# Performance work log

Measured on AMD Instinct MI355X. Metric: run time of the kernel, lower is better.

The kernel has to match this reference:

```python
import jax, jax.numpy as jnp
import numpy as np

D_MODEL = 1024
H = 16
D_K = D_MODEL // H


def setup_inputs() -> dict:
    key = jax.random.key(0)
    ks = jax.random.split(key, 12)
    B, S = 2, 2048
    q = jax.random.normal(ks[0], (B, S, D_MODEL), dtype=jnp.float32)
    k = jax.random.normal(ks[1], (B, S, D_MODEL), dtype=jnp.float32)
    v = jax.random.normal(ks[2], (B, S, D_MODEL), dtype=jnp.float32)
    mask = jax.random.randint(ks[3], (1, 1, S, S), 0, 2, dtype=jnp.int32)
    sc = 1.0 / np.sqrt(D_MODEL)
    wq = jax.random.uniform(ks[4], (D_MODEL, D_MODEL), jnp.float32, -sc, sc)
    bq = jax.random.uniform(ks[5], (D_MODEL,), jnp.float32, -sc, sc)
    wk = jax.random.uniform(ks[6], (D_MODEL, D_MODEL), jnp.float32, -sc, sc)
    bk = jax.random.uniform(ks[7], (D_MODEL,), jnp.float32, -sc, sc)
    wv = jax.random.uniform(ks[8], (D_MODEL, D_MODEL), jnp.float32, -sc, sc)
    bv = jax.random.uniform(ks[9], (D_MODEL,), jnp.float32, -sc, sc)
    wo = jax.random.uniform(ks[10], (D_MODEL, D_MODEL), jnp.float32, -sc, sc)
    bo = jax.random.uniform(ks[11], (D_MODEL,), jnp.float32, -sc, sc)
    return {"q": q, "k": k, "v": v, "mask": mask,
            "wq": wq, "bq": bq, "wk": wk, "bk": bk,
            "wv": wv, "bv": bv, "wo": wo, "bo": bo}


def reference(q, k, v, mask, wq, bq, wk, bk, wv, bv, wo, bo):
    B, S, _ = q.shape
    # linear projections (torch Linear: x @ W.T + b)
    query = q @ wq.T + bq
    key = k @ wk.T + bk
    value = v @ wv.T + bv
    # [B, S, D] -> [B, H, S, d_k]
    query = query.reshape(B, S, H, D_K).transpose(0, 2, 1, 3)
    key = key.reshape(B, S, H, D_K).transpose(0, 2, 1, 3)
    value = value.reshape(B, S, H, D_K).transpose(0, 2, 1, 3)
    scores = jnp.einsum('bhqd,bhkd->bhqk', query, key) / jnp.sqrt(
        jnp.asarray(D_K, query.dtype))
    # NOTE: source uses `-1 ** 9` which is -1 in Python, not -1e9 (soft mask)
    scores = jnp.where(mask == 0, jnp.asarray(-1.0, scores.dtype), scores)
    attn = jax.nn.softmax(scores, axis=-1)
    # source calls dropout(attn) but discards the result -> no-op
    x = jnp.einsum('bhqk,bhkd->bhqd', attn, value)
    x = x.transpose(0, 2, 1, 3).reshape(B, S, H * D_K)
    return x @ wo.T + bo
```

## Files before the change

kernel.cpp:

```cpp
#include <hip/hip_runtime.h>
#include <hip/hip_bf16.h>

#define D_MODEL 1024
#define NH 16
#define DK 64
#define S_LEN 2048
#define BATCH 2
#define M_ROWS (BATCH * S_LEN)

typedef float    floatx4 __attribute__((ext_vector_type(4)));
typedef _Float16 half8   __attribute__((ext_vector_type(8)));
typedef _Float16 half4v  __attribute__((ext_vector_type(4)));

__device__ __forceinline__ half8 ldh8(const _Float16* p) {
    return __builtin_bit_cast(half8, *(const uint4*)p);
}
__device__ __forceinline__ void gld16(const void* g, void* l) {
    __builtin_amdgcn_global_load_lds(
        (const __attribute__((address_space(1))) void*)g,
        (__attribute__((address_space(3))) void*)l, 16, 0, 0);
}

__global__ __launch_bounds__(256)
void cast_h(const float* __restrict__ s0, const float* __restrict__ s1,
            const float* __restrict__ s2, const float* __restrict__ s3,
            _Float16* __restrict__ out, int R) {
    const int z = blockIdx.y;
    const float* src = (z == 0) ? s0 : (z == 1) ? s1 : (z == 2) ? s2 : s3;
    const size_t idx = ((size_t)blockIdx.x * 256 + threadIdx.x) * 4;
    float4 v = *(const float4*)&src[idx];
    half4v h = {(_Float16)v.x, (_Float16)v.y, (_Float16)v.z, (_Float16)v.w};
    *(half4v*)&out[(size_t)z * R * 1024 + idx] = h;
}

template <int OUTMODE>
__global__ __launch_bounds__(256)
void gemm_f16(const _Float16* __restrict__ Abase, const _Float16* __restrict__ Wbase,
              const float* __restrict__ b0, const float* __restrict__ b1,
              const float* __restrict__ b2, void* __restrict__ Obase) {
    __shared__ __align__(16) _Float16 As[128 * 64];
    __shared__ __align__(16) _Float16 Ws[128 * 64];
    const int tid = threadIdx.x;
    const int w = tid >> 6, lane = tid & 63;
    const int l15 = lane & 15, q4 = lane >> 4;
    const int z = (OUTMODE == 1) ? blockIdx.z : 0;
    const int m0 = blockIdx.y * 128, n0 = blockIdx.x * 128;
    const int wm = w >> 1, wn = w & 1;

    const _Float16* A = Abase + (size_t)z * M_ROWS * 1024;
    const _Float16* W = Wbase + (size_t)z * 1024 * 1024;
    const float* bias = (OUTMODE == 1) ? ((z == 0) ? b0 : (z == 1) ? b1 : b2) : b0;

    int srow[4], sseg[4];
#pragma unroll
    for (int i = 0; i < 4; i++) {
        const int slot = i * 256 + tid;
        srow[i] = slot >> 3;
        sseg[i] = ((slot & 7) ^ (srow[i] & 7)) * 8;
    }

    int aoff[4][2], woff[4][2];
#pragma unroll
    for (int r = 0; r < 4; r++) {
        const int ar = wm * 64 + r * 16 + l15;
        const int wr = wn * 64 + r * 16 + l15;
#pragma unroll
        for (int kc = 0; kc < 2; kc++) {
            aoff[r][kc] = (ar * 8 + ((kc * 4 + q4) ^ (ar & 7))) * 8;
            woff[r][kc] = (wr * 8 + ((kc * 4 + q4) ^ (wr & 7))) * 8;
        }
    }

    floatx4 acc[4][4];
#pragma unroll
    for (int r = 0; r < 4; r++)
#pragma unroll
        for (int c = 0; c < 4; c++) acc[r][c] = (floatx4){0.f, 0.f, 0.f, 0.f};

    for (int k0 = 0; k0 < 1024; k0 += 64) {
#pragma unroll
        for (int i = 0; i < 4; i++) {
            const int lb = (i * 256 + w * 64) * 8;
            gld16(&A[(size_t)(m0 + srow[i]) * 1024 + k0 + sseg[i]], &As[lb]);
            gld16(&W[(size_t)(n0 + srow[i]) * 1024 + k0 + sseg[i]], &Ws[lb]);
        }
        __syncthreads();

        half8 af[4][2], wf[4][2];
#pragma unroll
        for (int r = 0; r < 4; r++)
#pragma unroll
            for (int kc = 0; kc < 2; kc++) {
                af[r][kc] = ldh8(&As[aoff[r][kc]]);
                wf[r][kc] = ldh8(&Ws[woff[r][kc]]);
            }
#pragma unroll
        for (int kc = 0; kc < 2; kc++)
#pragma unroll
            for (int r = 0; r < 4; r++)
#pragma unroll
                for (int c = 0; c < 4; c++)
                    acc[r][c] = __builtin_amdgcn_mfma_f32_16x16x32_f16(
                        af[r][kc], wf[c][kc], acc[r][c], 0, 0, 0);
        __syncthreads();
    }

#pragma unroll
    for (int r = 0; r < 4; r++)
#pragma unroll
        for (int c = 0; c < 4; c++)
#pragma unroll
            for (int reg = 0; reg < 4; reg++) {
                const int m = m0 + wm * 64 + r * 16 + q4 * 4 + reg;
                const int n = n0 + wn * 64 + c * 16 + l15;
                float val = acc[r][c][reg] + bias[n];
                if (OUTMODE == 0) {
                    ((float*)Obase)[(size_t)m * 1024 + n] = val;
                } else {
                    if (z == 0) val *= 0.125f;
                    const int b = m >> 11, s = m & 2047;
                    const int h = n >> 6, d = n & 63;
                    _Float16* Oz = (_Float16*)Obase + (size_t)z * M_ROWS * 1024;
                    Oz[(((size_t)(b * 16 + h) * S_LEN + s) << 6) + d] = (_Float16)val;
                }
            }
}

__global__ __launch_bounds__(256)
void vt_trans(const short* __restrict__ Vh, short* __restrict__ Vt) {
    __shared__ __align__(16) short T[64][80];
    const int bh = blockIdx.y;
    const int s0 = blockIdx.x * 64;
    const int t = threadIdx.x;
#pragma unroll
    for (int i = 0; i < 2; i++) {
        const int p = t + i * 256, r = p >> 3, c8 = (p & 7) * 8;
        uint4 raw = *(const uint4*)&Vh[((size_t)bh * S_LEN + s0 + r) * 64 + c8];
        const short* sv = (const short*)&raw;
#pragma unroll
        for (int j = 0; j < 8; j++) T[c8 + j][r] = sv[j];
    }
    __syncthreads();
#pragma unroll
    for (int i = 0; i < 2; i++) {
        const int p = t + i * 256, d = p >> 3, seg = (p & 7) * 8;
        *(uint4*)&Vt[((size_t)bh * DK + d) * S_LEN + s0 + seg] =
            *(const uint4*)&T[d][seg];
    }
}

__global__ __launch_bounds__(256)
void mask_pack(const int* __restrict__ mask, unsigned long long* __restrict__ mb) {
    const int gw = blockIdx.x * 4 + (threadIdx.x >> 6);
    const int lane = threadIdx.x & 63;
    const int row = gw >> 5, wid = gw & 31;
    const int mv = mask[(size_t)row * S_LEN + wid * 64 + lane];
    unsigned long long bal = __ballot(mv != 0);
    if (lane == 0) mb[gw] = bal;
}

__global__ __launch_bounds__(256)
void attn_mfma(const _Float16* __restrict__ Qh, const _Float16* __restrict__ Kh,
               const _Float16* __restrict__ Vt, const unsigned long long* __restrict__ mb,
               _Float16* __restrict__ Xh) {
    __shared__ __align__(16) _Float16 Ks[64 * 72];
    __shared__ __align__(16) _Float16 Vs[64 * 72];
    __shared__ __align__(16) _Float16 Ps[4][16 * 72];

    const int tid = threadIdx.x;
    const int w = tid >> 6, lane = tid & 63;
    const int l15 = lane & 15, q4 = lane >> 4;
    const int bh = blockIdx.y, b = bh >> 4, h = bh & 15;
    const int qb = blockIdx.x * 64 + w * 16;

    const _Float16* Qg = Qh + ((size_t)bh * S_LEN + qb) * DK;
    const _Float16* Kg = Kh + (size_t)bh * S_LEN * DK;
    const _Float16* Vg = Vt + (size_t)bh * DK * S_LEN;

    half8 Aq[2];
#pragma unroll
    for (int c = 0; c < 2; c++)
        Aq[c] = ldh8(&Qg[l15 * DK + c * 32 + q4 * 8]);

    floatx4 O[4];
#pragma unroll
    for (int nt = 0; nt < 4; nt++) O[nt] = (floatx4){0.f, 0.f, 0.f, 0.f};
    float lsum[4] = {0.f, 0.f, 0.f, 0.f};

    for (int j0 = 0; j0 < S_LEN; j0 += 64) {
#pragma unroll
        for (int i = 0; i < 2; i++) {
            int p = tid + i * 256, r = p >> 3, seg = (p & 7) * 8;
            *(uint4*)&Ks[r * 72 + seg] = *(const uint4*)&Kg[(size_t)(j0 + r) * DK + seg];
            *(uint4*)&Vs[r * 72 + seg] = *(const uint4*)&Vg[(size_t)r * S_LEN + j0 + seg];
        }
        unsigned long long mw[4];
#pragma unroll
        for (int reg = 0; reg < 4; reg++)
            mw[reg] = mb[(size_t)(qb + q4 * 4 + reg) * (S_LEN / 64) + (j0 >> 6)];
        __syncthreads();

        floatx4 Sf[4];
#pragma unroll
        for (int jt = 0; jt < 4; jt++) {
            floatx4 c = {0.f, 0.f, 0.f, 0.f};
#pragma unroll
            for (int ch = 0; ch < 2; ch++) {
                half8 bk = ldh8(&Ks[(jt * 16 + l15) * 72 + ch * 32 + q4 * 8]);
                c = __builtin_amdgcn_mfma_f32_16x16x32_f16(Aq[ch], bk, c, 0, 0, 0);
            }
            Sf[jt] = c;
        }

#pragma unroll
        for (int reg = 0; reg < 4; reg++) {
#pragma unroll
            for (int jt = 0; jt < 4; jt++) {
                float s = Sf[jt][reg];
                s = ((mw[reg] >> (jt * 16 + l15)) & 1ull) ? s : -1.0f;
                float p = __expf(s);
                lsum[reg] += p;
                Ps[w][(q4 * 4 + reg) * 72 + jt * 16 + l15] = (_Float16)p;
            }
        }

        half8 Ap[2];
#pragma unroll
        for (int ch = 0; ch < 2; ch++)
            Ap[ch] = ldh8(&Ps[w][l15 * 72 + ch * 32 + q4 * 8]);
#pragma unroll
        for (int nt = 0; nt < 4; nt++) {
#pragma unroll
            for (int ch = 0; ch < 2; ch++) {
                half8 bv = ldh8(&Vs[(nt * 16 + l15) * 72 + ch * 32 + q4 * 8]);
                O[nt] = __builtin_amdgcn_mfma_f32_16x16x32_f16(Ap[ch], bv, O[nt], 0, 0, 0);
            }
        }
        __syncthreads();
    }

#pragma unroll
    for (int reg = 0; reg < 4; reg++) {
#pragma unroll
        for (int off = 1; off < 16; off <<= 1)
            lsum[reg] += __shfl_xor(lsum[reg], off, 64);
    }
#pragma unroll
    for (int reg = 0; reg < 4; reg++) {
        const float inv = 1.0f / lsum[reg];
        const int srow = qb + q4 * 4 + reg;
#pragma unroll
        for (int nt = 0; nt < 4; nt++)
            Xh[((size_t)(b * S_LEN + srow)) * 1024 + h * DK + nt * 16 + l15] =
                (_Float16)(O[nt][reg] * inv);
    }
}

extern "C" void kernel_launch(void* const* d_in, const int* in_sizes, int n_in,
                              void* d_out, int out_size, void* d_ws, size_t ws_size,
                              hipStream_t stream) {
    const float* q  = (const float*)d_in[0];
    const float* k  = (const float*)d_in[1];
    const float* v  = (const float*)d_in[2];
    const int* mask = (const int*)d_in[3];
    const float* wq = (const float*)d_in[4];
    const float* bq = (const float*)d_in[5];
    const float* wk = (const float*)d_in[6];
    const float* bk = (const float*)d_in[7];
    const float* wv = (const float*)d_in[8];
    const float* bv = (const float*)d_in[9];
    const float* wo = (const float*)d_in[10];
    const float* bo = (const float*)d_in[11];
    float* out = (float*)d_out;

    char* ws = (char*)d_ws;
    const size_t MB = 1u << 20;
    _Float16* Wh   = (_Float16*)ws;
    _Float16* Ah   = (_Float16*)(ws + 8 * MB);
    _Float16* QKVh = (_Float16*)(ws + 32 * MB);
    _Float16* Vt   = (_Float16*)(ws + 56 * MB);
    unsigned long long* mb = (unsigned long long*)(ws + 64 * MB);
    _Float16* Xh   = Ah;

    cast_h<<<dim3(1024, 4), 256, 0, stream>>>(wq, wk, wv, wo, Wh, 1024);
    cast_h<<<dim3(4096, 3), 256, 0, stream>>>(q, k, v, nullptr, Ah, M_ROWS);

    gemm_f16<1><<<dim3(8, 32, 3), 256, 0, stream>>>(Ah, Wh, bq, bk, bv, QKVh);

    vt_trans<<<dim3(32, 32), 256, 0, stream>>>(
        (const short*)(QKVh + (size_t)2 * M_ROWS * 1024), (short*)Vt);
    mask_pack<<<S_LEN * (S_LEN / 64) / 4, 256, 0, stream>>>(mask, mb);

    attn_mfma<<<dim3(32, 32), 256, 0, stream>>>(QKVh, QKVh + (size_t)M_ROWS * 1024,
                                                Vt, mb, Xh);

    gemm_f16<0><<<dim3(8, 32, 1), 256, 0, stream>>>(Xh, Wh + (size_t)3 * 1024 * 1024,
                                                    bo, bo, bo, out);
}
```

Measured before the change: 299.5 us.

## Restructure attention: 32 query rows per wave, direct K/V register loads, exp2 softmax

The attention kernel now gives each wave 32 query rows, so every K/V fragment is reused across two query subtiles, and the grid is halved. K and V fragments are loaded straight from global memory into registers, which drops the shared-memory staging and both block-level barriers. The Q projection folds log2(e) into its scale so the softmax can use the hardware exp2, and P is written to LDS as packed half2 pairs exchanged via DPP. The costs are more registers per wave, fewer blocks in flight, and K/V global loads repeated by each of the four waves instead of shared.

```diff
diff --git a/kernel.cpp b/kernel.cpp
--- a/kernel.cpp
+++ b/kernel.cpp
@@ -11,6 +11,9 @@
 typedef float    floatx4 __attribute__((ext_vector_type(4)));
 typedef _Float16 half8   __attribute__((ext_vector_type(8)));
 typedef _Float16 half4v  __attribute__((ext_vector_type(4)));
+typedef _Float16 half2v  __attribute__((ext_vector_type(2)));
+
+#define LOG2E 1.4426950408889634f
 
 __device__ __forceinline__ half8 ldh8(const _Float16* p) {
     return __builtin_bit_cast(half8, *(const uint4*)p);
@@ -19,6 +22,10 @@
     __builtin_amdgcn_global_load_lds(
         (const __attribute__((address_space(1))) void*)g,
         (__attribute__((address_space(3))) void*)l, 16, 0, 0);
+}
+__device__ __forceinline__ float dpp_swap1(float x) {
+    return __builtin_bit_cast(float,
+        __builtin_amdgcn_mov_dpp(__builtin_bit_cast(int, x), 0xB1, 0xF, 0xF, false));
 }
 
 __global__ __launch_bounds__(256)
@@ -117,7 +124,7 @@
                 if (OUTMODE == 0) {
                     ((float*)Obase)[(size_t)m * 1024 + n] = val;
                 } else {
-                    if (z == 0) val *= 0.125f;
+                    if (z == 0) val *= 0.125f * LOG2E;
                     const int b = m >> 11, s = m & 2047;
                     const int h = n >> 6, d = n & 63;
                     _Float16* Oz = (_Float16*)Obase + (size_t)z * M_ROWS * 1024;
@@ -163,97 +170,123 @@
 void attn_mfma(const _Float16* __restrict__ Qh, const _Float16* __restrict__ Kh,
                const _Float16* __restrict__ Vt, const unsigned long long* __restrict__ mb,
                _Float16* __restrict__ Xh) {
-    __shared__ __align__(16) _Float16 Ks[64 * 72];
-    __shared__ __align__(16) _Float16 Vs[64 * 72];
-    __shared__ __align__(16) _Float16 Ps[4][16 * 72];
+    __shared__ __align__(16) _Float16 Ps[4][32 * 72];
 
     const int tid = threadIdx.x;
     const int w = tid >> 6, lane = tid & 63;
     const int l15 = lane & 15, q4 = lane >> 4;
     const int bh = blockIdx.y, b = bh >> 4, h = bh & 15;
-    const int qb = blockIdx.x * 64 + w * 16;
+    const int qb = blockIdx.x * 128 + w * 32;
 
     const _Float16* Qg = Qh + ((size_t)bh * S_LEN + qb) * DK;
     const _Float16* Kg = Kh + (size_t)bh * S_LEN * DK;
     const _Float16* Vg = Vt + (size_t)bh * DK * S_LEN;
 
-    half8 Aq[2];
-#pragma unroll
-    for (int c = 0; c < 2; c++)
-        Aq[c] = ldh8(&Qg[l15 * DK + c * 32 + q4 * 8]);
-
-    floatx4 O[4];
-#pragma unroll
-    for (int nt = 0; nt < 4; nt++) O[nt] = (floatx4){0.f, 0.f, 0.f, 0.f};
-    float lsum[4] = {0.f, 0.f, 0.f, 0.f};
+    half8 Aq[2][2];
+#pragma unroll
+    for (int qs = 0; qs < 2; qs++)
+#pragma unroll
+        for (int ch = 0; ch < 2; ch++)
+            Aq[qs][ch] = ldh8(&Qg[(qs * 16 + l15) * DK + ch * 32 + q4 * 8]);
+
+    int mrow[2][4];
+#pragma unroll
+    for (int qs = 0; qs < 2; qs++)
+#pragma unroll
+        for (int reg = 0; reg < 4; reg++)
+            mrow[qs][reg] = (qb + qs * 16 + q4 * 4 + reg) * (S_LEN / 64);
+
+    floatx4 O[2][4];
+#pragma unroll
+    for (int qs = 0; qs < 2; qs++)
+#pragma unroll
+        for (int nt = 0; nt < 4; nt++) O[qs][nt] = (floatx4){0.f, 0.f, 0.f, 0.f};
+    float lsum[2][4] = {{0.f, 0.f, 0.f, 0.f}, {0.f, 0.f, 0.f, 0.f}};
+
+    const bool evenlane = ((lane & 1) == 0);
 
     for (int j0 = 0; j0 < S_LEN; j0 += 64) {
-#pragma unroll
-        for (int i = 0; i < 2; i++) {
-            int p = tid + i * 256, r = p >> 3, seg = (p & 7) * 8;
-            *(uint4*)&Ks[r * 72 + seg] = *(const uint4*)&Kg[(size_t)(j0 + r) * DK + seg];
-            *(uint4*)&Vs[r * 72 + seg] = *(const uint4*)&Vg[(size_t)r * S_LEN + j0 + seg];
-        }
-        unsigned long long mw[4];
-#pragma unroll
-        for (int reg = 0; reg < 4; reg++)
-            mw[reg] = mb[(size_t)(qb + q4 * 4 + reg) * (S_LEN / 64) + (j0 >> 6)];
-        __syncthreads();
-
-        floatx4 Sf[4];
-#pragma unroll
-        for (int jt = 0; jt < 4; jt++) {
-            floatx4 c = {0.f, 0.f, 0.f, 0.f};
-#pragma unroll
-            for (int ch = 0; ch < 2; ch++) {
-                half8 bk = ldh8(&Ks[(jt * 16 + l15) * 72 + ch * 32 + q4 * 8]);
-                c = __builtin_amdgcn_mfma_f32_16x16x32_f16(Aq[ch], bk, c, 0, 0, 0);
-            }
-            Sf[jt] = c;
-        }
-
+        half8 Kf[4][2];
+#pragma unroll
+        for (int jt = 0; jt < 4; jt++)
+#pragma unroll
+            for (int ch = 0; ch < 2; ch++)
+                Kf[jt][ch] = ldh8(&Kg[(size_t)(j0 + jt * 16 + l15) * DK +
+                                      ch * 32 + q4 * 8]);
+        half8 bv[4][2];
+#pragma unroll
+        for (int nt = 0; nt < 4; nt++)
+#pragma unroll
+            for (int ch = 0; ch < 2; ch++)
+                bv[nt][ch] = ldh8(&Vg[(size_t)(nt * 16 + l15) * S_LEN + j0 +
+                                      ch * 32 + q4 * 8]);
+        const int jw = j0 >> 6;
+
+#pragma unroll
+        for (int qs = 0; qs < 2; qs++) {
+            floatx4 Sf[4];
+#pragma unroll
+            for (int jt = 0; jt < 4; jt++) {
+                floatx4 c = (floatx4){0.f, 0.f, 0.f, 0.f};
+                c = __builtin_amdgcn_mfma_f32_16x16x32_f16(Aq[qs][0], Kf[jt][0], c, 0, 0, 0);
+                c = __builtin_amdgcn_mfma_f32_16x16x32_f16(Aq[qs][1], Kf[jt][1], c, 0, 0, 0);
+                Sf[jt] = c;
+            }
+#pragma unroll
+            for (int reg = 0; reg < 4; reg++) {
+                const unsigned long long m = mb[mrow[qs][reg] + jw];
+#pragma unroll
+                for (int jt = 0; jt < 4; jt++) {
+                    float s = Sf[jt][reg];
+                    s = ((m >> (jt * 16 + l15)) & 1ull) ? s : -LOG2E;
+                    const float p = __builtin_amdgcn_exp2f(s);
+                    lsum[qs][reg] += p;
+                    const float po = dpp_swap1(p);
+                    if (evenlane) {
+                        *(unsigned*)&Ps[w][(qs * 16 + q4 * 4 + reg) * 72 +
+                                           jt * 16 + l15] =
+                            __builtin_bit_cast(unsigned,
+                                __builtin_amdgcn_cvt_pkrtz(p, po));
+                    }
+                }
+            }
+        }
+
+#pragma unroll
+        for (int qs = 0; qs < 2; qs++) {
+            half8 Ap[2];
+#pragma unroll
+            for (int ch = 0; ch < 2; ch++)
+                Ap[ch] = ldh8(&Ps[w][(qs * 16 + l15) * 72 + ch * 32 + q4 * 8]);
+#pragma unroll
+            for (int nt = 0; nt < 4; nt++) {
+                O[qs][nt] = __builtin_amdgcn_mfma_f32_16x16x32_f16(
+                    Ap[0], bv[nt][0], O[qs][nt], 0, 0, 0);
+                O[qs][nt] = __builtin_amdgcn_mfma_f32_16x16x32_f16(
+                    Ap[1], bv[nt][1], O[qs][nt], 0, 0, 0);
+            }
+        }
+    }
+
+#pragma unroll
+    for (int qs = 0; qs < 2; qs++)
 #pragma unroll
         for (int reg = 0; reg < 4; reg++) {
 #pragma unroll
-            for (int jt = 0; jt < 4; jt++) {
-                float s = Sf[jt][reg];
-                s = ((mw[reg] >> (jt * 16 + l15)) & 1ull) ? s : -1.0f;
-                float p = __expf(s);
-                lsum[reg] += p;
-                Ps[w][(q4 * 4 + reg) * 72 + jt * 16 + l15] = (_Float16)p;
-            }
-        }
-
-        half8 Ap[2];
-#pragma unroll
-        for (int ch = 0; ch < 2; ch++)
-            Ap[ch] = ldh8(&Ps[w][l15 * 72 + ch * 32 + q4 * 8]);
-#pragma unroll
-        for (int nt = 0; nt < 4; nt++) {
-#pragma unroll
-            for (int ch = 0; ch < 2; ch++) {
-                half8 bv = ldh8(&Vs[(nt * 16 + l15) * 72 + ch * 32 + q4 * 8]);
-                O[nt] = __builtin_amdgcn_mfma_f32_16x16x32_f16(Ap[ch], bv, O[nt], 0, 0, 0);
-            }
-        }
-        __syncthreads();
-    }
-
-#pragma unroll
-    for (int reg = 0; reg < 4; reg++) {
-#pragma unroll
-        for (int off = 1; off < 16; off <<= 1)
-            lsum[reg] += __shfl_xor(lsum[reg], off, 64);
-    }
-#pragma unroll
-    for (int reg = 0; reg < 4; reg++) {
-        const float inv = 1.0f / lsum[reg];
-        const int srow = qb + q4 * 4 + reg;
-#pragma unroll
-        for (int nt = 0; nt < 4; nt++)
-            Xh[((size_t)(b * S_LEN + srow)) * 1024 + h * DK + nt * 16 + l15] =
-                (_Float16)(O[nt][reg] * inv);
-    }
+            for (int off = 1; off < 16; off <<= 1)
+                lsum[qs][reg] += __shfl_xor(lsum[qs][reg], off, 64);
+        }
+#pragma unroll
+    for (int qs = 0; qs < 2; qs++)
+#pragma unroll
+        for (int reg = 0; reg < 4; reg++) {
+            const float inv = 1.0f / lsum[qs][reg];
+            const int srow = qb + qs * 16 + q4 * 4 + reg;
+            _Float16* Xrow = Xh + (size_t)(b * S_LEN + srow) * 1024 + h * DK;
+#pragma unroll
+            for (int nt = 0; nt < 4; nt++)
+                Xrow[nt * 16 + l15] = (_Float16)(O[qs][nt][reg] * inv);
+        }
 }
 
 extern "C" void kernel_launch(void* const* d_in, const int* in_sizes, int n_in,
@@ -291,7 +324,7 @@
         (const short*)(QKVh + (size_t)2 * M_ROWS * 1024), (short*)Vt);
     mask_pack<<<S_LEN * (S_LEN / 64) / 4, 256, 0, stream>>>(mask, mb);
 
-    attn_mfma<<<dim3(32, 32), 256, 0, stream>>>(QKVh, QKVh + (size_t)M_ROWS * 1024,
+    attn_mfma<<<dim3(16, 32), 256, 0, stream>>>(QKVh, QKVh + (size_t)M_ROWS * 1024,
                                                 Vt, mb, Xh);
 
     gemm_f16<0><<<dim3(8, 32, 1), 256, 0, stream>>>(Xh, Wh + (size_t)3 * 1024 * 1024,
```

Measured after the change: 385.3 us. 28.7% more time.
